# Kernel tuning notes

Hardware: AMD Instinct MI355X
Metric: run time of the kernel (lower is better)

## Reference

```python
import jax, jax.numpy as jnp
import numpy as np

HEADS = 8
GROUPS = 32   # Group_cnt in the source
WIN = 16      # config.local_window_size


def _gn_nc(x, groups, eps):
    # group_norm on [N, C] (affine=False)
    N, C = x.shape
    xg = x.reshape(N, groups, C // groups)
    m = xg.mean(axis=2, keepdims=True)
    v = xg.var(axis=2, keepdims=True)
    return ((xg - m) / jnp.sqrt(v + eps)).reshape(N, C)


def _gn_nchw(x, groups, eps):
    # group_norm on [B, C, H, W] (affine=False)
    B, C, H, W = x.shape
    xg = x.reshape(B, groups, C // groups, H, W)
    m = xg.mean(axis=(2, 3, 4), keepdims=True)
    v = xg.var(axis=(2, 3, 4), keepdims=True)
    return ((xg - m) / jnp.sqrt(v + eps)).reshape(B, C, H, W)


def _conv3x3(x, w, b=None):
    y = jax.lax.conv_general_dilated(x, w, (1, 1), 'SAME',
                                     dimension_numbers=('NCHW', 'OIHW', 'NCHW'))
    return y if b is None else y + b[None, :, None, None]


def _forward(x, temb, conv1_w, conv1_b, conv2_w, g_diff, g_res, g2, g3,
             qkv2_w, qkv2_b, out2_w, qkv3_w, qkv3_b, out3_w,
             lsa_qkv_w, lsa_out_w):
    # ---- Residual_Block (layer1) ----
    h = _gn_nchw(x, GROUPS, 1e-6)
    h = _conv3x3(h, conv1_w, conv1_b)
    h = h + g_diff * temb[:, :, None, None]      # gate_diffusion (ReZero-style gate)
    h = jax.nn.silu(h)
    h = _gn_nchw(h, GROUPS, 1e-6)
    h = _conv3x3(h, conv2_w)
    h = _gn_nchw(h, GROUPS, 1e-6)
    x = x + g_res * h                            # gate_residual

    B, C, Fq, T = x.shape
    Dh = C // HEADS
    scale = 1.0 / jnp.sqrt(jnp.float32(Dh))      # (F/heads)**0.5 divisor

    # ---- SelfAttention over frequency axis (layer2): batch B*T, seq Fq ----
    xf = x.transpose(0, 3, 2, 1).reshape(B * T, Fq, C)
    qkv = xf @ qkv2_w + qkv2_b                   # [B*T, Fq, 3C]
    q, k, v = [t.reshape(B * T, Fq, HEADS, Dh) for t in jnp.split(qkv, 3, axis=-1)]
    p = jax.nn.softmax(jnp.einsum('bLhf,blhf->bLlh', q, k) * scale, axis=2)
    y = jnp.einsum('blhf,bLlh->bLhf', v, p).reshape(B * T, Fq, C) @ out2_w
    y = _gn_nc(y.reshape(-1, C), GROUPS, 1e-5).reshape(B * T, Fq, C)
    xf = xf + g2 * y                             # gate2

    # ---- GlobalAttention over time axis (layer3): batch B*Fq, seq T ----
    xt = xf.reshape(B, T, Fq, C).transpose(0, 2, 1, 3).reshape(B * Fq, T, C)
    qkv = xt @ qkv3_w + qkv3_b
    q, k, v = [t.reshape(B * Fq, T, HEADS, Dh) for t in jnp.split(qkv, 3, axis=-1)]
    p = jax.nn.softmax(jnp.einsum('bhf,blhf->blh', q.mean(axis=1), k) * scale, axis=1)
    y = jnp.einsum('blhf,blh->bhf', v, p).reshape(B * Fq, C) @ out3_w
    y = _gn_nc(y, GROUPS, 1e-5).reshape(B * Fq, 1, C)
    xt = xt + g3 * y                             # gate3, broadcast over T
    x = xt.reshape(B, Fq, T, C).transpose(0, 3, 1, 2)

    # ---- LSA_block (layer4): pre-norm local windowed attention along T, residual ----
    h = _gn_nchw(x, GROUPS, 1e-5)
    h = h.transpose(0, 2, 3, 1).reshape(B * Fq, T, C)
    nw = T // WIN
    qkv = (h @ lsa_qkv_w).reshape(B * Fq, nw, WIN, 3 * C)
    q, k, v = [t.reshape(B * Fq, nw, WIN, HEADS, Dh) for t in jnp.split(qkv, 3, axis=-1)]
    p = jax.nn.softmax(jnp.einsum('nwqhd,nwkhd->nwqkh', q, k) * scale, axis=3)
    o = jnp.einsum('nwqkh,nwkhd->nwqhd', p, v).reshape(B * Fq, T, C) @ lsa_out_w
    return x + o.reshape(B, Fq, T, C).transpose(0, 3, 1, 2)


def setup_inputs() -> dict:
    key = jax.random.key(0)
    ks = jax.random.split(key, 10)
    B, C, Fq, T = 4, 256, 64, 256
    w = lambda k, s: jax.random.normal(k, s, dtype=jnp.float32) * 0.02
    return {
        'x': jax.random.normal(ks[0], (B, C, Fq, T), dtype=jnp.float32),
        'temb': jax.random.normal(ks[1], (B, C), dtype=jnp.float32),
        'conv1_w': w(ks[2], (C, C, 3, 3)),
        'conv1_b': jnp.zeros((C,), jnp.float32),
        'conv2_w': w(ks[3], (C, C, 3, 3)),
        'g_diff': jnp.full((1,), 0.5, jnp.float32),
        'g_res': jnp.full((1,), 0.5, jnp.float32),
        'g2': jnp.full((1,), 0.5, jnp.float32),
        'g3': jnp.full((1,), 0.5, jnp.float32),
        'qkv2_w': w(ks[4], (C, 3 * C)),
        'qkv2_b': jnp.zeros((3 * C,), jnp.float32),
        'out2_w': w(ks[5], (C, C)),
        'qkv3_w': w(ks[6], (C, 3 * C)),
        'qkv3_b': jnp.zeros((3 * C,), jnp.float32),
        'out3_w': w(ks[7], (C, C)),
        'lsa_qkv_w': w(ks[8], (C, 3 * C)),
        'lsa_out_w': w(ks[9], (C, C)),
    }


def reference(x, temb, conv1_w, conv1_b, conv2_w, g_diff, g_res, g2, g3,
              qkv2_w, qkv2_b, out2_w, qkv3_w, qkv3_b, out3_w,
              lsa_qkv_w, lsa_out_w):
    return _forward(x, temb, conv1_w, conv1_b, conv2_w, g_diff, g_res, g2, g3,
                    qkv2_w, qkv2_b, out2_w, qkv3_w, qkv3_b, out3_w,
                    lsa_qkv_w, lsa_out_w)
```

## Files before the change

### kernel.cpp

```cpp
#include <hip/hip_runtime.h>

#define NN 16777216
#define CC 256
#define FF 64
#define TT 256

typedef short v8s __attribute__((ext_vector_type(8)));
typedef float v4f __attribute__((ext_vector_type(4)));

__device__ __forceinline__ unsigned short f2bf(float f) {
  unsigned u = __float_as_uint(f);
  u += 0x7fff + ((u >> 16) & 1);
  return (unsigned short)(u >> 16);
}
__device__ __forceinline__ float bf2f(unsigned short h) {
  return __uint_as_float(((unsigned)h) << 16);
}
__device__ __forceinline__ unsigned packbf2(float a, float b) {
  return (unsigned)f2bf(a) | ((unsigned)f2bf(b) << 16);
}
__device__ __forceinline__ void unpack8(uint4 u, float* d) {
  d[0] = __uint_as_float(u.x << 16); d[1] = __uint_as_float(u.x & 0xffff0000u);
  d[2] = __uint_as_float(u.y << 16); d[3] = __uint_as_float(u.y & 0xffff0000u);
  d[4] = __uint_as_float(u.z << 16); d[5] = __uint_as_float(u.z & 0xffff0000u);
  d[6] = __uint_as_float(u.w << 16); d[7] = __uint_as_float(u.w & 0xffff0000u);
}

__device__ __forceinline__ void blockReduce2(float& a, float& b, float* sbuf) {
  #pragma unroll
  for (int off = 32; off > 0; off >>= 1) {
    a += __shfl_down(a, off, 64);
    b += __shfl_down(b, off, 64);
  }
  int w = threadIdx.x >> 6;
  if ((threadIdx.x & 63) == 0) { sbuf[w] = a; sbuf[4 + w] = b; }
  __syncthreads();
  if (threadIdx.x == 0) {
    a = sbuf[0] + sbuf[1] + sbuf[2] + sbuf[3];
    b = sbuf[4] + sbuf[5] + sbuf[6] + sbuf[7];
  }
}

__global__ void prep_all_k(const float* __restrict__ c1w, const float* __restrict__ c2w,
    const float* __restrict__ q2w, const float* __restrict__ o2w, const float* __restrict__ q3w,
    const float* __restrict__ lqw, const float* __restrict__ low,
    unsigned short* __restrict__ WB1, unsigned short* __restrict__ WB2,
    unsigned short* __restrict__ Q2T, unsigned short* __restrict__ O2T,
    unsigned short* __restrict__ Q3T, unsigned short* __restrict__ LQT,
    unsigned short* __restrict__ LOT, float* __restrict__ stats) {
  long s = (long)blockIdx.x * 256 + threadIdx.x;
  if (s < 1024) { stats[s] = 0.f; return; }
  s -= 1024;
  if (s < 589824) {
    int co = (int)(s / 2304), r = (int)(s % 2304);
    int ci = r / 9, tap = r % 9;
    WB1[(tap * 256 + co) * 256 + ci] = f2bf(c1w[s]);
    return;
  }
  s -= 589824;
  if (s < 589824) {
    int co = (int)(s / 2304), r = (int)(s % 2304);
    int ci = r / 9, tap = r % 9;
    WB2[(tap * 256 + co) * 256 + ci] = f2bf(c2w[s]);
    return;
  }
  s -= 589824;
  if (s < 196608) { int k = (int)(s / 768), n = (int)(s % 768); Q2T[n * 256 + k] = f2bf(q2w[s]); return; }
  s -= 196608;
  if (s < 65536)  { int k = (int)(s / 256), n = (int)(s % 256); O2T[n * 256 + k] = f2bf(o2w[s]); return; }
  s -= 65536;
  if (s < 196608) { int k = (int)(s / 768), n = (int)(s % 768); Q3T[n * 256 + k] = f2bf(q3w[s]); return; }
  s -= 196608;
  if (s < 196608) { int k = (int)(s / 768), n = (int)(s % 768); LQT[n * 256 + k] = f2bf(lqw[s]); return; }
  s -= 196608;
  if (s < 65536)  { int k = (int)(s / 256), n = (int)(s % 256); LOT[n * 256 + k] = f2bf(low[s]); return; }
}

__global__ __launch_bounds__(256) void gn_stats_contig(const float* __restrict__ src, float* __restrict__ stats) {
  __shared__ float sbuf[8];
  int grp = blockIdx.x >> 3, chunk = blockIdx.x & 7;
  const float4* p = (const float4*)src + grp * 32768 + chunk * 4096;
  float s = 0.f, ss = 0.f;
  for (int i = threadIdx.x; i < 4096; i += 256) {
    float4 v = p[i];
    s += v.x + v.y + v.z + v.w;
    ss += v.x * v.x + v.y * v.y + v.z * v.z + v.w * v.w;
  }
  blockReduce2(s, ss, sbuf);
  if (threadIdx.x == 0) { atomicAdd(&stats[grp], s); atomicAdd(&stats[128 + grp], ss); }
}

__global__ __launch_bounds__(256) void gn_apply_tr_k(const float* __restrict__ src,
    const float* __restrict__ stats, unsigned short* __restrict__ XC, float eps) {
  __shared__ float sT[32][33];
  int bx = blockIdx.x;
  int r = bx >> 6;
  int c0 = ((bx >> 3) & 7) * 32;
  int t0 = (bx & 7) * 32;
  int b = r >> 6, f = r & 63;
  int tl = threadIdx.x & 31, tr = threadIdx.x >> 5;
  #pragma unroll
  for (int i = 0; i < 4; ++i) {
    int c = c0 + tr + i * 8;
    int grp = b * 32 + (c >> 3);
    float mean = stats[grp] * (1.f / 131072.f);
    float var = stats[128 + grp] * (1.f / 131072.f) - mean * mean;
    float rv = rsqrtf(var + eps);
    float v = src[((b * 256 + c) * 64 + f) * 256 + t0 + tl];
    sT[tr + i * 8][tl] = (v - mean) * rv;
  }
  __syncthreads();
  #pragma unroll
  for (int i = 0; i < 4; ++i) {
    int t = t0 + tr + i * 8;
    XC[(((size_t)(b * 64 + f)) * 256 + t) * 256 + c0 + tl] = f2bf(sT[tl][tr + i * 8]);
  }
}

__global__ __launch_bounds__(256) void gn_tr_resid_k(const float* __restrict__ h,
    const float* __restrict__ x, const float* __restrict__ stats,
    const float* __restrict__ gate, float* __restrict__ XF, float eps) {
  __shared__ float sT[32][33];
  int bx = blockIdx.x;
  int r = bx >> 6;
  int c0 = ((bx >> 3) & 7) * 32;
  int t0 = (bx & 7) * 32;
  int b = r >> 6, f = r & 63;
  int tl = threadIdx.x & 31, tr = threadIdx.x >> 5;
  float g = gate[0];
  #pragma unroll
  for (int i = 0; i < 4; ++i) {
    int c = c0 + tr + i * 8;
    int grp = b * 32 + (c >> 3);
    float mean = stats[grp] * (1.f / 131072.f);
    float var = stats[128 + grp] * (1.f / 131072.f) - mean * mean;
    float rv = rsqrtf(var + eps);
    int idx = ((b * 256 + c) * 64 + f) * 256 + t0 + tl;
    sT[tr + i * 8][tl] = x[idx] + g * (h[idx] - mean) * rv;
  }
  __syncthreads();
  #pragma unroll
  for (int i = 0; i < 4; ++i) {
    int t = t0 + tr + i * 8;
    XF[(((size_t)(b * 256 + t)) * 64 + f) * 256 + c0 + tl] = sT[tl][tr + i * 8];
  }
}

__global__ __launch_bounds__(256, 4) void conv3x3_mfma_k(const unsigned short* __restrict__ XC,
    const unsigned short* __restrict__ wb, const float* __restrict__ bias,
    const float* __restrict__ temb, const float* __restrict__ gd,
    float* __restrict__ out, float* __restrict__ ostats, int mode) {
  __shared__ __align__(16) unsigned short sIn[258][40];
  __shared__ __align__(16) unsigned short sW[3][64][40];
  int f  = blockIdx.x;
  int b  = blockIdx.y >> 2;
  int co0 = (blockIdx.y & 3) * 64;
  int tid = threadIdx.x;
  int wave = tid >> 6, lane = tid & 63;
  int lm = lane & 15, quad = lane >> 4;
  int w64 = wave * 64;
  v4f acc[4][4];
  #pragma unroll
  for (int i = 0; i < 4; ++i)
    #pragma unroll
    for (int j = 0; j < 4; ++j) acc[i][j] = (v4f)(0.f);

  for (int ci0 = 0; ci0 < 256; ci0 += 32) {
    for (int df = 0; df < 3; ++df) {
      __syncthreads();
      for (int s = tid; s < 1032; s += 256) {
        int tl = s >> 2, part = s & 3;
        int fi = f + df - 1, tg = tl - 1;
        uint4 val = make_uint4(0, 0, 0, 0);
        if (fi >= 0 && fi < 64 && tg >= 0 && tg < 256)
          val = *(const uint4*)&XC[(((size_t)(b * 64 + fi)) * 256 + tg) * 256 + ci0 + part * 8];
        *(uint4*)&sIn[tl][part * 8] = val;
      }
      for (int s = tid; s < 768; s += 256) {
        int tap3 = s >> 8, r = s & 255;
        int co = r >> 2, part = r & 3;
        *(uint4*)&sW[tap3][co][part * 8] =
            *(const uint4*)&wb[((size_t)((df * 3 + tap3) * 256) + co0 + co) * 256 + ci0 + part * 8];
      }
      __syncthreads();
      #pragma unroll
      for (int dt = 0; dt < 3; ++dt) {
        v8s A[4];
        #pragma unroll
        for (int mt = 0; mt < 4; ++mt)
          A[mt] = *(const v8s*)&sIn[w64 + mt * 16 + lm + dt][quad * 8];
        #pragma unroll
        for (int nt = 0; nt < 4; ++nt) {
          v8s B = *(const v8s*)&sW[dt][nt * 16 + lm][quad * 8];
          #pragma unroll
          for (int mt = 0; mt < 4; ++mt)
            acc[mt][nt] = __builtin_amdgcn_mfma_f32_16x16x32_bf16(A[mt], B, acc[mt][nt], 0, 0, 0);
        }
      }
    }
  }
  __syncthreads();
  float* sStat = (float*)sIn;
  float gdv = mode ? gd[0] : 0.f;
  float sch, qch;
  #pragma unroll
  for (int nt = 0; nt < 4; ++nt) {
    int co = co0 + nt * 16 + lm;
    float bb = 0.f;
    if (mode) bb = bias[co] + gdv * temb[b * 256 + co];
    sch = 0.f; qch = 0.f;
    #pragma unroll
    for (int mt = 0; mt < 4; ++mt) {
      int t = w64 + mt * 16 + quad * 4;
      float v0 = acc[mt][nt][0] + bb, v1 = acc[mt][nt][1] + bb;
      float v2 = acc[mt][nt][2] + bb, v3 = acc[mt][nt][3] + bb;
      if (mode) {
        v0 = v0 / (1.f + expf(-v0)); v1 = v1 / (1.f + expf(-v1));
        v2 = v2 / (1.f + expf(-v2)); v3 = v3 / (1.f + expf(-v3));
      }
      float4 o; o.x = v0; o.y = v1; o.z = v2; o.w = v3;
      *(float4*)&out[(((size_t)b * 256 + co) * 64 + f) * 256 + t] = o;
      sch += v0 + v1 + v2 + v3;
      qch += v0 * v0 + v1 * v1 + v2 * v2 + v3 * v3;
    }
    sch += __shfl_xor(sch, 16); qch += __shfl_xor(qch, 16);
    sch += __shfl_xor(sch, 32); qch += __shfl_xor(qch, 32);
    if (quad == 0) {
      sStat[((wave * 4 + nt) * 16 + lm) * 2]     = sch;
      sStat[((wave * 4 + nt) * 16 + lm) * 2 + 1] = qch;
    }
  }
  __syncthreads();
  if (tid < 64) {
    int c = tid;
    int nt = c >> 4, lmm = c & 15;
    float s = 0.f, q = 0.f;
    #pragma unroll
    for (int w = 0; w < 4; ++w) {
      s += sStat[((w * 4 + nt) * 16 + lmm) * 2];
      q += sStat[((w * 4 + nt) * 16 + lmm) * 2 + 1];
    }
    s += __shfl_xor(s, 1); q += __shfl_xor(q, 1);
    s += __shfl_xor(s, 2); q += __shfl_xor(q, 2);
    s += __shfl_xor(s, 4); q += __shfl_xor(q, 4);
    if ((c & 7) == 0) {
      int g = (co0 + c) >> 3;
      atomicAdd(&ostats[b * 32 + g], s);
      atomicAdd(&ostats[128 + b * 32 + g], q);
    }
  }
}

__global__ __launch_bounds__(256) void gemm_af32_k(const float* __restrict__ A, int lda,
    const unsigned short* __restrict__ BT, const float* __restrict__ bias,
    unsigned short* __restrict__ Cb, int ldc,
    const float* __restrict__ gstats, int growbase, float eps) {
  __shared__ __align__(16) unsigned short sA[128][40];
  __shared__ __align__(16) unsigned short sB[128][40];
  int n0 = blockIdx.x * 128, m0 = blockIdx.y * 128;
  int tid = threadIdx.x;
  int wave = tid >> 6, lane = tid & 63;
  int wm = wave >> 1, wn = wave & 1;
  int lm = lane & 15, quad = lane >> 4;
  v4f acc[4][4];
  #pragma unroll
  for (int i = 0; i < 4; ++i)
    #pragma unroll
    for (int j = 0; j < 4; ++j) acc[i][j] = (v4f)(0.f);

  for (int k0 = 0; k0 < 256; k0 += 32) {
    __syncthreads();
    #pragma unroll
    for (int i = 0; i < 4; ++i) {
      int s = tid + i * 256;
      int row = s >> 3, k4 = s & 7;
      float4 av = *(const float4*)&A[(size_t)(m0 + row) * lda + k0 + k4 * 4];
      if (gstats) {
        int grp = ((growbase + m0 + row) >> 14) * 32 + ((k0 + k4 * 4) >> 3);
        float mean = gstats[grp] * (1.f / 131072.f);
        float var = gstats[128 + grp] * (1.f / 131072.f) - mean * mean;
        float rr = rsqrtf(var + eps);
        av.x = (av.x - mean) * rr; av.y = (av.y - mean) * rr;
        av.z = (av.z - mean) * rr; av.w = (av.w - mean) * rr;
      }
      *(uint2*)&sA[row][k4 * 4] = make_uint2(packbf2(av.x, av.y), packbf2(av.z, av.w));
    }
    #pragma unroll
    for (int i = 0; i < 2; ++i) {
      int s = tid + i * 256;
      int n = s >> 2, part = s & 3;
      *(uint4*)&sB[n][part * 8] = *(const uint4*)&BT[(size_t)(n0 + n) * 256 + k0 + part * 8];
    }
    __syncthreads();
    v8s Af[4];
    #pragma unroll
    for (int mt = 0; mt < 4; ++mt)
      Af[mt] = *(const v8s*)&sA[wm * 64 + mt * 16 + lm][quad * 8];
    #pragma unroll
    for (int nt = 0; nt < 4; ++nt) {
      v8s Bf = *(const v8s*)&sB[wn * 64 + nt * 16 + lm][quad * 8];
      #pragma unroll
      for (int mt = 0; mt < 4; ++mt)
        acc[mt][nt] = __builtin_amdgcn_mfma_f32_16x16x32_bf16(Af[mt], Bf, acc[mt][nt], 0, 0, 0);
    }
  }
  #pragma unroll
  for (int nt = 0; nt < 4; ++nt) {
    int col = n0 + wn * 64 + nt * 16 + lm;
    float bb = bias ? bias[col] : 0.f;
    #pragma unroll
    for (int mt = 0; mt < 4; ++mt) {
      int row = m0 + wm * 64 + mt * 16 + quad * 4;
      #pragma unroll
      for (int r = 0; r < 4; ++r)
        Cb[(size_t)(row + r) * ldc + col] = f2bf(acc[mt][nt][r] + bb);
    }
  }
}

__global__ __launch_bounds__(256) void gemm_abf16_k(const unsigned short* __restrict__ A, int lda,
    const unsigned short* __restrict__ BT,
    const float* __restrict__ xfin, float* __restrict__ xtout, int rowbase,
    unsigned short* __restrict__ Cb, int ldc, const float* __restrict__ gate, int mode) {
  __shared__ __align__(16) unsigned short sA[128][40];
  __shared__ __align__(16) unsigned short sB[128][40];
  int n0 = blockIdx.x * 128, m0 = blockIdx.y * 128;
  int tid = threadIdx.x;
  int wave = tid >> 6, lane = tid & 63;
  int wm = wave >> 1, wn = wave & 1;
  int lm = lane & 15, quad = lane >> 4;
  v4f acc[4][4];
  #pragma unroll
  for (int i = 0; i < 4; ++i)
    #pragma unroll
    for (int j = 0; j < 4; ++j) acc[i][j] = (v4f)(0.f);

  for (int k0 = 0; k0 < 256; k0 += 32) {
    __syncthreads();
    #pragma unroll
    for (int i = 0; i < 2; ++i) {
      int s = tid + i * 256;
      int row = s >> 2, part = s & 3;
      *(uint4*)&sA[row][part * 8] = *(const uint4*)&A[(size_t)(m0 + row) * lda + k0 + part * 8];
      *(uint4*)&sB[row][part * 8] = *(const uint4*)&BT[(size_t)(n0 + row) * 256 + k0 + part * 8];
    }
    __syncthreads();
    v8s Af[4];
    #pragma unroll
    for (int mt = 0; mt < 4; ++mt)
      Af[mt] = *(const v8s*)&sA[wm * 64 + mt * 16 + lm][quad * 8];
    #pragma unroll
    for (int nt = 0; nt < 4; ++nt) {
      v8s Bf = *(const v8s*)&sB[wn * 64 + nt * 16 + lm][quad * 8];
      #pragma unroll
      for (int mt = 0; mt < 4; ++mt)
        acc[mt][nt] = __builtin_amdgcn_mfma_f32_16x16x32_bf16(Af[mt], Bf, acc[mt][nt], 0, 0, 0);
    }
  }
  if (mode == 1) {
    float g = gate[0];
    #pragma unroll
    for (int mt = 0; mt < 4; ++mt) {
      int rowb = m0 + wm * 64 + mt * 16 + quad * 4;
      #pragma unroll
      for (int r = 0; r < 4; ++r) {
        int rowl = rowb + r;
        int rowg = rowbase + rowl;
        int b = rowg >> 14, t = (rowg >> 6) & 255, fq = rowg & 63;
        size_t xtrow = (size_t)((b * 64 + fq) * 256 + t) * 256;
        #pragma unroll
        for (int nt = 0; nt < 4; ++nt) {
          float v = acc[mt][nt][r];
          float s = v, q = v * v;
          s += __shfl_xor(s, 1); q += __shfl_xor(q, 1);
          s += __shfl_xor(s, 2); q += __shfl_xor(q, 2);
          s += __shfl_xor(s, 4); q += __shfl_xor(q, 4);
          float m = s * 0.125f;
          float var = q * 0.125f - m * m;
          float norm = (v - m) * rsqrtf(var + 1e-5f);
          int col = n0 + wn * 64 + nt * 16 + lm;
          xtout[xtrow + col] = xfin[(size_t)rowl * 256 + col] + g * norm;
        }
      }
    }
  } else if (mode == 2) {
    #pragma unroll
    for (int mt = 0; mt < 4; ++mt) {
      int rowb = m0 + wm * 64 + mt * 16 + quad * 4;
      #pragma unroll
      for (int r = 0; r < 4; ++r) {
        int rowl = rowb + r;
        int rowg = rowbase + rowl;
        int b = rowg >> 14, fq = (rowg >> 8) & 63, t = rowg & 255;
        #pragma unroll
        for (int nt = 0; nt < 4; ++nt) {
          int col = n0 + wn * 64 + nt * 16 + lm;
          float v = acc[mt][nt][r] + xfin[(size_t)rowl * 256 + col];
          xtout[(((size_t)b * 256 + col) * 64 + fq) * 256 + t] = v;
        }
      }
    }
  } else {
    #pragma unroll
    for (int nt = 0; nt < 4; ++nt) {
      int col = n0 + wn * 64 + nt * 16 + lm;
      #pragma unroll
      for (int mt = 0; mt < 4; ++mt) {
        int row = m0 + wm * 64 + mt * 16 + quad * 4;
        #pragma unroll
        for (int r = 0; r < 4; ++r)
          Cb[(size_t)(row + r) * ldc + col] = f2bf(acc[mt][nt][r]);
      }
    }
  }
}

__global__ __launch_bounds__(256) void gemm_k(const float* __restrict__ A, int lda,
    const float* __restrict__ Bm, int N, const float* __restrict__ bias,
    float* __restrict__ Cm, int ldc, int gn) {
  __shared__ __align__(16) float sA[16][64];
  __shared__ __align__(16) float sB[16][64];
  int n0 = blockIdx.x * 64, m0 = blockIdx.y * 64;
  int tid = threadIdx.x;
  int tx = tid & 15, ty = tid >> 4;
  int arow = m0 + (tid >> 2), acol = (tid & 3) * 4;
  int brow = tid >> 4, bcol = (tid & 15) * 4;
  float acc[4][4] = {};
  for (int k0 = 0; k0 < 256; k0 += 16) {
    __syncthreads();
    float4 av = *(const float4*)&A[(size_t)arow * lda + k0 + acol];
    sA[acol + 0][tid >> 2] = av.x;
    sA[acol + 1][tid >> 2] = av.y;
    sA[acol + 2][tid >> 2] = av.z;
    sA[acol + 3][tid >> 2] = av.w;
    *(float4*)&sB[brow][bcol] = *(const float4*)&Bm[(k0 + brow) * N + n0 + bcol];
    __syncthreads();
    #pragma unroll
    for (int kk = 0; kk < 16; ++kk) {
      float4 a = *(const float4*)&sA[kk][ty * 4];
      float4 b = *(const float4*)&sB[kk][tx * 4];
      float aa[4] = {a.x, a.y, a.z, a.w};
      float bb[4] = {b.x, b.y, b.z, b.w};
      #pragma unroll
      for (int i = 0; i < 4; ++i)
        #pragma unroll
        for (int j = 0; j < 4; ++j)
          acc[i][j] += aa[i] * bb[j];
    }
  }
  #pragma unroll
  for (int i = 0; i < 4; ++i) {
    float m = 0.f, rv = 1.f;
    if (gn) {
      float s = acc[i][0] + acc[i][1] + acc[i][2] + acc[i][3];
      float q = acc[i][0] * acc[i][0] + acc[i][1] * acc[i][1]
              + acc[i][2] * acc[i][2] + acc[i][3] * acc[i][3];
      s += __shfl_xor(s, 1); q += __shfl_xor(q, 1);
      m = s * 0.125f;
      float var = q * 0.125f - m * m;
      rv = rsqrtf(var + 1e-5f);
    }
    #pragma unroll
    for (int j = 0; j < 4; ++j) {
      int n = n0 + tx * 4 + j;
      float v = acc[i][j];
      if (gn) v = (v - m) * rv;
      else if (bias) v += bias[n];
      Cm[(size_t)(m0 + ty * 4 + i) * ldc + n] = v;
    }
  }
}

__global__ __launch_bounds__(256) void attn2_mfma_k(unsigned short* __restrict__ Q) {
  __shared__ __align__(16) unsigned short sP[4][64][72];
  __shared__ __align__(16) unsigned short sVt[4][32][72];
  int bt = blockIdx.x;
  int tid = threadIdx.x;
  int wave = tid >> 6, lane = tid & 63;
  int lm = lane & 15, quad = lane >> 4;
  const float scale = 0.17677669529663687f;
  size_t rowbase = (size_t)bt * 64;
  unsigned short (*P)[72] = sP[wave];
  unsigned short (*Vt)[72] = sVt[wave];
  #pragma unroll
  for (int hh = 0; hh < 2; ++hh) {
    int h = wave * 2 + hh;
    int hoff = h * 32;
    v8s Af[4], Bf[4];
    #pragma unroll
    for (int mt = 0; mt < 4; ++mt)
      Af[mt] = *(const v8s*)&Q[(rowbase + mt * 16 + lm) * 768 + hoff + quad * 8];
    #pragma unroll
    for (int nt = 0; nt < 4; ++nt)
      Bf[nt] = *(const v8s*)&Q[(rowbase + nt * 16 + lm) * 768 + 256 + hoff + quad * 8];
    v4f S[4][4];
    #pragma unroll
    for (int mt = 0; mt < 4; ++mt)
      #pragma unroll
      for (int nt = 0; nt < 4; ++nt)
        S[mt][nt] = __builtin_amdgcn_mfma_f32_16x16x32_bf16(Af[mt], Bf[nt], (v4f)(0.f), 0, 0, 0);
    #pragma unroll
    for (int part = 0; part < 4; ++part) {
      uint4 u = *(const uint4*)&Q[(rowbase + lane) * 768 + 512 + hoff + part * 8];
      unsigned short* up = (unsigned short*)&u;
      #pragma unroll
      for (int j = 0; j < 8; ++j) Vt[part * 8 + j][lane] = up[j];
    }
    float inv[4][4];
    #pragma unroll
    for (int mt = 0; mt < 4; ++mt) {
      #pragma unroll
      for (int r = 0; r < 4; ++r) {
        float v0 = S[mt][0][r] * scale, v1 = S[mt][1][r] * scale;
        float v2 = S[mt][2][r] * scale, v3 = S[mt][3][r] * scale;
        float mx = fmaxf(fmaxf(v0, v1), fmaxf(v2, v3));
        mx = fmaxf(mx, __shfl_xor(mx, 1));
        mx = fmaxf(mx, __shfl_xor(mx, 2));
        mx = fmaxf(mx, __shfl_xor(mx, 4));
        mx = fmaxf(mx, __shfl_xor(mx, 8));
        float e0 = __expf(v0 - mx), e1 = __expf(v1 - mx);
        float e2 = __expf(v2 - mx), e3 = __expf(v3 - mx);
        float sm = e0 + e1 + e2 + e3;
        sm += __shfl_xor(sm, 1);
        sm += __shfl_xor(sm, 2);
        sm += __shfl_xor(sm, 4);
        sm += __shfl_xor(sm, 8);
        inv[mt][r] = 1.f / sm;
        int row = mt * 16 + quad * 4 + r;
        P[row][lm]      = f2bf(e0);
        P[row][16 + lm] = f2bf(e1);
        P[row][32 + lm] = f2bf(e2);
        P[row][48 + lm] = f2bf(e3);
      }
    }
    v8s Ap[4][2], Bv[2][2];
    #pragma unroll
    for (int mt = 0; mt < 4; ++mt)
      #pragma unroll
      for (int kc = 0; kc < 2; ++kc)
        Ap[mt][kc] = *(const v8s*)&P[mt * 16 + lm][kc * 32 + quad * 8];
    #pragma unroll
    for (int nd = 0; nd < 2; ++nd)
      #pragma unroll
      for (int kc = 0; kc < 2; ++kc)
        Bv[nd][kc] = *(const v8s*)&Vt[nd * 16 + lm][kc * 32 + quad * 8];
    #pragma unroll
    for (int mt = 0; mt < 4; ++mt) {
      #pragma unroll
      for (int nd = 0; nd < 2; ++nd) {
        v4f O = (v4f)(0.f);
        O = __builtin_amdgcn_mfma_f32_16x16x32_bf16(Ap[mt][0], Bv[nd][0], O, 0, 0, 0);
        O = __builtin_amdgcn_mfma_f32_16x16x32_bf16(Ap[mt][1], Bv[nd][1], O, 0, 0, 0);
        #pragma unroll
        for (int r = 0; r < 4; ++r)
          P[mt * 16 + quad * 4 + r][nd * 16 + lm] = f2bf(O[r] * inv[mt][r]);
      }
    }
    #pragma unroll
    for (int part = 0; part < 4; ++part) {
      uint4 u = *(const uint4*)&P[lane][part * 8];
      *(uint4*)&Q[(rowbase + lane) * 768 + hoff + part * 8] = u;
    }
  }
}

__global__ __launch_bounds__(256) void attn3_k(const unsigned short* __restrict__ Q3,
                                               float* __restrict__ y3, int bf_base) {
  __shared__ float sQp[64][33];
  __shared__ float sqm[32];
  __shared__ float sp[256];
  __shared__ float sred[256];
  int bfl = blockIdx.x >> 3, h = blockIdx.x & 7;
  int tid = threadIdx.x;
  int tq = tid >> 2, c4 = tid & 3;
  int d8 = c4 * 8;
  const float scale = 0.17677669529663687f;
  size_t rowbase = (size_t)bfl * 256;
  {
    float a[8] = {};
    #pragma unroll
    for (int i = 0; i < 4; ++i) {
      int t = i * 64 + tq;
      float v[8];
      unpack8(*(const uint4*)&Q3[(rowbase + t) * 768 + h * 32 + d8], v);
      #pragma unroll
      for (int j = 0; j < 8; ++j) a[j] += v[j];
    }
    #pragma unroll
    for (int j = 0; j < 8; ++j) sQp[tq][d8 + j] = a[j];
  }
  __syncthreads();
  if (tid < 32) {
    float m = 0.f;
    for (int g = 0; g < 64; ++g) m += sQp[g][tid];
    sqm[tid] = m * (1.f / 256.f);
  }
  __syncthreads();
  {
    float dot = 0.f;
    #pragma unroll
    for (int p = 0; p < 4; ++p) {
      float v[8];
      unpack8(*(const uint4*)&Q3[(rowbase + tid) * 768 + 256 + h * 32 + p * 8], v);
      #pragma unroll
      for (int j = 0; j < 8; ++j) dot += sqm[p * 8 + j] * v[j];
    }
    sp[tid] = dot * scale;
    sred[tid] = sp[tid];
  }
  __syncthreads();
  for (int st = 128; st > 0; st >>= 1) { if (tid < st) sred[tid] = fmaxf(sred[tid], sred[tid + st]); __syncthreads(); }
  float mx = sred[0];
  __syncthreads();
  float e = expf(sp[tid] - mx);
  sred[tid] = e;
  __syncthreads();
  for (int st = 128; st > 0; st >>= 1) { if (tid < st) sred[tid] += sred[tid + st]; __syncthreads(); }
  float rinv = 1.f / sred[0];
  sp[tid] = e * rinv;
  __syncthreads();
  {
    float a[8] = {};
    #pragma unroll
    for (int i = 0; i < 4; ++i) {
      int t = i * 64 + tq;
      float w = sp[t];
      float v[8];
      unpack8(*(const uint4*)&Q3[(rowbase + t) * 768 + 512 + h * 32 + d8], v);
      #pragma unroll
      for (int j = 0; j < 8; ++j) a[j] += w * v[j];
    }
    #pragma unroll
    for (int j = 0; j < 8; ++j) sQp[tq][d8 + j] = a[j];
  }
  __syncthreads();
  if (tid < 32) {
    float o = 0.f;
    for (int g = 0; g < 64; ++g) o += sQp[g][tid];
    y3[(size_t)(bf_base + bfl) * 256 + h * 32 + tid] = o;
  }
}

__global__ __launch_bounds__(256) void lsa_attn_k(unsigned short* __restrict__ Q4) {
  __shared__ __align__(16) float sX[16][772];
  __shared__ float sS[8][16][17];
  __shared__ float sInv[8][16];
  int bfl = blockIdx.x >> 4, w = blockIdx.x & 15;
  int tid = threadIdx.x;
  size_t rb = ((size_t)(bfl * 256 + w * 16)) * 768;
  for (int s = tid; s < 1536; s += 256) {
    int t = s / 96, c8 = (s - t * 96) * 8;
    unpack8(*(const uint4*)&Q4[rb + t * 768 + c8], &sX[t][c8]);
  }
  __syncthreads();
  const float scale = 0.17677669529663687f;
  #pragma unroll
  for (int rep = 0; rep < 8; ++rep) {
    int idx = tid + rep * 256;
    int h = idx >> 8, q = (idx >> 4) & 15, k = idx & 15;
    float dot = 0.f;
    const float* qp = &sX[q][h * 32];
    const float* kp = &sX[k][256 + h * 32];
    for (int d = 0; d < 32; ++d) dot += qp[d] * kp[d];
    sS[h][q][k] = dot * scale;
  }
  __syncthreads();
  if (tid < 128) {
    int h = tid >> 4, q = tid & 15;
    float mx = -1e30f;
    for (int k = 0; k < 16; ++k) mx = fmaxf(mx, sS[h][q][k]);
    float sum = 0.f;
    for (int k = 0; k < 16; ++k) { float e = expf(sS[h][q][k] - mx); sS[h][q][k] = e; sum += e; }
    sInv[h][q] = 1.f / sum;
  }
  __syncthreads();
  #pragma unroll
  for (int rep = 0; rep < 8; ++rep) {
    int idx = tid + rep * 256;
    int t = idx >> 7, c2 = (idx & 127) * 2;
    int h = c2 >> 5;
    float a0 = 0.f, a1 = 0.f;
    for (int k = 0; k < 16; ++k) {
      float p = sS[h][t][k];
      a0 += p * sX[k][512 + c2];
      a1 += p * sX[k][512 + c2 + 1];
    }
    float riv = sInv[h][t];
    *(unsigned*)&Q4[rb + t * 768 + c2] = packbf2(a0 * riv, a1 * riv);
  }
}

__global__ __launch_bounds__(256) void bcast_add_k(float* __restrict__ XT, const float* __restrict__ y3n,
                                                   const float* __restrict__ gate) {
  int i4 = blockIdx.x * 256 + threadIdx.x;
  int flat = i4 * 4;
  int r = flat >> 16, c = flat & 255;
  float g = gate[0];
  float4 v = ((float4*)XT)[i4];
  float4 a = *(const float4*)&y3n[r * 256 + c];
  v.x += g * a.x; v.y += g * a.y; v.z += g * a.z; v.w += g * a.w;
  ((float4*)XT)[i4] = v;
}

__global__ __launch_bounds__(256) void gn_stats_xt2_k(const float* __restrict__ X, float* __restrict__ stats) {
  __shared__ float sacc[4][64];
  int bf = blockIdx.x >> 1, half = blockIdx.x & 1;
  int b = bf >> 6;
  int tid = threadIdx.x;
  const float4* p = (const float4*)X + (size_t)bf * 16384 + half * 8192;
  float s = 0.f, q = 0.f;
  #pragma unroll 4
  for (int k = 0; k < 32; ++k) {
    float4 v = p[tid + k * 256];
    s += v.x + v.y + v.z + v.w;
    q += v.x * v.x + v.y * v.y + v.z * v.z + v.w * v.w;
  }
  s += __shfl_xor(s, 1); q += __shfl_xor(q, 1);
  int lane = tid & 63, wave = tid >> 6;
  if ((lane & 1) == 0) {
    int g = (lane >> 1) & 31;
    sacc[wave][g * 2] = s;
    sacc[wave][g * 2 + 1] = q;
  }
  __syncthreads();
  if (tid < 64) {
    int g = tid >> 1, isq = tid & 1;
    float acc = sacc[0][g * 2 + isq] + sacc[1][g * 2 + isq]
              + sacc[2][g * 2 + isq] + sacc[3][g * 2 + isq];
    atomicAdd(&stats[isq * 128 + b * 32 + g], acc);
  }
}

extern "C" void kernel_launch(void* const* d_in, const int* in_sizes, int n_in,
                              void* d_out, int out_size, void* d_ws, size_t ws_size,
                              hipStream_t stream) {
  (void)in_sizes; (void)n_in; (void)out_size;
  const float* x        = (const float*)d_in[0];
  const float* temb     = (const float*)d_in[1];
  const float* conv1_w  = (const float*)d_in[2];
  const float* conv1_b  = (const float*)d_in[3];
  const float* conv2_w  = (const float*)d_in[4];
  const float* g_diff   = (const float*)d_in[5];
  const float* g_res    = (const float*)d_in[6];
  const float* g2       = (const float*)d_in[7];
  const float* g3       = (const float*)d_in[8];
  const float* qkv2_w   = (const float*)d_in[9];
  const float* qkv2_b   = (const float*)d_in[10];
  const float* out2_w   = (const float*)d_in[11];
  const float* qkv3_w   = (const float*)d_in[12];
  const float* qkv3_b   = (const float*)d_in[13];
  const float* out3_w   = (const float*)d_in[14];
  const float* lsa_qkv_w = (const float*)d_in[15];
  const float* lsa_out_w = (const float*)d_in[16];
  float* out = (float*)d_out;
  float* ws = (float*)d_ws;

  int NCHv = 4;
  {
    auto need = [](int nch) -> size_t {
      size_t rows = 65536 / nch;
      size_t uslots = rows * 512;
      if (uslots < 8388608) uslots = 8388608;
      return 4ull * ((size_t)NN + uslots + 950272 + 198000);
    };
    if (ws_size >= need(1)) NCHv = 1;
    else if (ws_size >= need(2)) NCHv = 2;
  }
  const size_t rows = 65536 / NCHv;

  float* W = ws;
  float* U = ws + (size_t)NN;
  unsigned short* XC  = (unsigned short*)U;
  unsigned short* QB  = (unsigned short*)U;
  size_t uslots = rows * 512; if (uslots < 8388608) uslots = 8388608;
  float* WREG = U + uslots;
  unsigned short* WB1   = (unsigned short*)WREG;
  unsigned short* WB2   = WB1 + 589824;
  unsigned short* QKV2T = WB2 + 589824;
  unsigned short* OUT2T = QKV2T + 196608;
  unsigned short* QKV3T = OUT2T + 65536;
  unsigned short* LSAQT = QKV3T + 196608;
  unsigned short* LSAOT = LSAQT + 196608;
  float* Y3    = WREG + 950272;
  float* Y3O   = Y3 + 65536;
  float* Y3N   = Y3O + 65536;
  float* STATS = Y3N + 65536;
  float* ST0 = STATS, *ST1 = STATS + 256, *ST2 = STATS + 512, *ST3 = STATS + 768;
  float* D = out;

  dim3 b256(256);
  prep_all_k<<<7428, b256, 0, stream>>>(conv1_w, conv2_w, qkv2_w, out2_w, qkv3_w,
                                        lsa_qkv_w, lsa_out_w,
                                        WB1, WB2, QKV2T, OUT2T, QKV3T, LSAQT, LSAOT, STATS);

  gn_stats_contig<<<1024, b256, 0, stream>>>(x, ST0);
  gn_apply_tr_k<<<16384, b256, 0, stream>>>(x, ST0, XC, 1e-6f);
  conv3x3_mfma_k<<<dim3(64, 16), b256, 0, stream>>>(XC, WB1, conv1_b, temb, g_diff, W, ST1, 1);
  gn_apply_tr_k<<<16384, b256, 0, stream>>>(W, ST1, XC, 1e-6f);
  conv3x3_mfma_k<<<dim3(64, 16), b256, 0, stream>>>(XC, WB2, nullptr, nullptr, nullptr, W, ST2, 0);
  gn_tr_resid_k<<<16384, b256, 0, stream>>>(W, x, ST2, g_res, D, 1e-6f);

  for (int c = 0; c < NCHv; ++c) {
    float* XFr = D + (size_t)c * rows * 256;
    gemm_af32_k<<<dim3(6, rows / 128), b256, 0, stream>>>(XFr, 256, QKV2T, qkv2_b, QB, 768, nullptr, 0, 0.f);
    attn2_mfma_k<<<rows / 64, b256, 0, stream>>>(QB);
    gemm_abf16_k<<<dim3(2, rows / 128), b256, 0, stream>>>(QB, 768, OUT2T,
                                                           XFr, W, (int)(c * rows),
                                                           nullptr, 256, g2, 1);
  }

  for (int c = 0; c < NCHv; ++c) {
    const float* XTr = W + (size_t)c * rows * 256;
    gemm_af32_k<<<dim3(6, rows / 128), b256, 0, stream>>>(XTr, 256, QKV3T, qkv3_b, QB, 768, nullptr, 0, 0.f);
    attn3_k<<<(rows / 256) * 8, b256, 0, stream>>>(QB, Y3, c * (int)(rows / 256));
  }
  gemm_k<<<dim3(4, 4), b256, 0, stream>>>(Y3, 256, out3_w, 256, nullptr, Y3N, 256, 1);
  bcast_add_k<<<16384, b256, 0, stream>>>(W, Y3N, g3);

  gn_stats_xt2_k<<<512, b256, 0, stream>>>(W, ST3);
  for (int c = 0; c < NCHv; ++c) {
    const float* XTr = W + (size_t)c * rows * 256;
    gemm_af32_k<<<dim3(6, rows / 128), b256, 0, stream>>>(XTr, 256, LSAQT, nullptr, QB, 768,
                                                          ST3, (int)(c * rows), 1e-5f);
    lsa_attn_k<<<(rows / 256) * 16, b256, 0, stream>>>(QB);
    gemm_abf16_k<<<dim3(2, rows / 128), b256, 0, stream>>>(QB, 768, LSAOT,
                                                           XTr, out, (int)(c * rows),
                                                           nullptr, 256, nullptr, 2);
  }
}
```

Before: 1.005 ms.

## Fuse query column-sum into QKV3 GEMM epilogue and merge broadcast-add with GN stats

The QKV3 GEMM now accumulates per-sequence query column sums with atomics in its epilogue and skips writing the Q block to memory, so attn3 reads the precomputed mean instead of rereading 256 Q rows. Separately, the gated broadcast add and the group-norm statistics pass over the time-major tensor are merged into one kernel, which removes one full read/write sweep of the 64 MB buffer. This adds atomic contention on qsum and relies on the mean-only use of Q in attn3.

```diff
diff --git a/kernel.cpp b/kernel.cpp
--- a/kernel.cpp
+++ b/kernel.cpp
@@ -47,7 +47,8 @@
     unsigned short* __restrict__ WB1, unsigned short* __restrict__ WB2,
     unsigned short* __restrict__ Q2T, unsigned short* __restrict__ O2T,
     unsigned short* __restrict__ Q3T, unsigned short* __restrict__ LQT,
-    unsigned short* __restrict__ LOT, float* __restrict__ stats) {
+    unsigned short* __restrict__ LOT, float* __restrict__ stats,
+    float* __restrict__ qsum) {
   long s = (long)blockIdx.x * 256 + threadIdx.x;
   if (s < 1024) { stats[s] = 0.f; return; }
   s -= 1024;
@@ -74,6 +75,8 @@
   if (s < 196608) { int k = (int)(s / 768), n = (int)(s % 768); LQT[n * 256 + k] = f2bf(lqw[s]); return; }
   s -= 196608;
   if (s < 65536)  { int k = (int)(s / 256), n = (int)(s % 256); LOT[n * 256 + k] = f2bf(low[s]); return; }
+  s -= 65536;
+  if (s < 65536)  { qsum[s] = 0.f; }
 }
 
 __global__ __launch_bounds__(256) void gn_stats_contig(const float* __restrict__ src, float* __restrict__ stats) {
@@ -254,7 +257,8 @@
 __global__ __launch_bounds__(256) void gemm_af32_k(const float* __restrict__ A, int lda,
     const unsigned short* __restrict__ BT, const float* __restrict__ bias,
     unsigned short* __restrict__ Cb, int ldc,
-    const float* __restrict__ gstats, int growbase, float eps) {
+    const float* __restrict__ gstats, int growbase, float eps,
+    float* __restrict__ qsum, int qrowbase) {
   __shared__ __align__(16) unsigned short sA[128][40];
   __shared__ __align__(16) unsigned short sB[128][40];
   int n0 = blockIdx.x * 128, m0 = blockIdx.y * 128;
@@ -304,16 +308,36 @@
         acc[mt][nt] = __builtin_amdgcn_mfma_f32_16x16x32_bf16(Af[mt], Bf, acc[mt][nt], 0, 0, 0);
     }
   }
-  #pragma unroll
-  for (int nt = 0; nt < 4; ++nt) {
-    int col = n0 + wn * 64 + nt * 16 + lm;
-    float bb = bias ? bias[col] : 0.f;
-    #pragma unroll
-    for (int mt = 0; mt < 4; ++mt) {
-      int row = m0 + wm * 64 + mt * 16 + quad * 4;
-      #pragma unroll
-      for (int r = 0; r < 4; ++r)
-        Cb[(size_t)(row + r) * ldc + col] = f2bf(acc[mt][nt][r] + bb);
+  if (qsum && n0 < 256) {
+    #pragma unroll
+    for (int nt = 0; nt < 4; ++nt) {
+      int col = n0 + wn * 64 + nt * 16 + lm;
+      float bb = bias ? bias[col] : 0.f;
+      float cs = 0.f;
+      #pragma unroll
+      for (int mt = 0; mt < 4; ++mt)
+        #pragma unroll
+        for (int r = 0; r < 4; ++r)
+          cs += acc[mt][nt][r] + bb;
+      cs += __shfl_xor(cs, 16);
+      cs += __shfl_xor(cs, 32);
+      if (quad == 0) {
+        int qrow = (qrowbase + m0) >> 8;
+        atomicAdd(&qsum[(size_t)qrow * 256 + col], cs);
+      }
+    }
+  } else {
+    #pragma unroll
+    for (int nt = 0; nt < 4; ++nt) {
+      int col = n0 + wn * 64 + nt * 16 + lm;
+      float bb = bias ? bias[col] : 0.f;
+      #pragma unroll
+      for (int mt = 0; mt < 4; ++mt) {
+        int row = m0 + wm * 64 + mt * 16 + quad * 4;
+        #pragma unroll
+        for (int r = 0; r < 4; ++r)
+          Cb[(size_t)(row + r) * ldc + col] = f2bf(acc[mt][nt][r] + bb);
+      }
     }
   }
 }
@@ -565,6 +589,7 @@
 }
 
 __global__ __launch_bounds__(256) void attn3_k(const unsigned short* __restrict__ Q3,
+                                               const float* __restrict__ qsum,
                                                float* __restrict__ y3, int bf_base) {
   __shared__ float sQp[64][33];
   __shared__ float sqm[32];
@@ -576,25 +601,8 @@
   int d8 = c4 * 8;
   const float scale = 0.17677669529663687f;
   size_t rowbase = (size_t)bfl * 256;
-  {
-    float a[8] = {};
-    #pragma unroll
-    for (int i = 0; i < 4; ++i) {
-      int t = i * 64 + tq;
-      float v[8];
-      unpack8(*(const uint4*)&Q3[(rowbase + t) * 768 + h * 32 + d8], v);
-      #pragma unroll
-      for (int j = 0; j < 8; ++j) a[j] += v[j];
-    }
-    #pragma unroll
-    for (int j = 0; j < 8; ++j) sQp[tq][d8 + j] = a[j];
-  }
-  __syncthreads();
-  if (tid < 32) {
-    float m = 0.f;
-    for (int g = 0; g < 64; ++g) m += sQp[g][tid];
-    sqm[tid] = m * (1.f / 256.f);
-  }
+  if (tid < 32)
+    sqm[tid] = qsum[(size_t)(bf_base + bfl) * 256 + h * 32 + tid] * (1.f / 256.f);
   __syncthreads();
   {
     float dot = 0.f;
@@ -690,44 +698,39 @@
   }
 }
 
-__global__ __launch_bounds__(256) void bcast_add_k(float* __restrict__ XT, const float* __restrict__ y3n,
-                                                   const float* __restrict__ gate) {
-  int i4 = blockIdx.x * 256 + threadIdx.x;
-  int flat = i4 * 4;
-  int r = flat >> 16, c = flat & 255;
-  float g = gate[0];
-  float4 v = ((float4*)XT)[i4];
-  float4 a = *(const float4*)&y3n[r * 256 + c];
-  v.x += g * a.x; v.y += g * a.y; v.z += g * a.z; v.w += g * a.w;
-  ((float4*)XT)[i4] = v;
-}
-
-__global__ __launch_bounds__(256) void gn_stats_xt2_k(const float* __restrict__ X, float* __restrict__ stats) {
+__global__ __launch_bounds__(256) void bcast_stats_k(float* __restrict__ XT, const float* __restrict__ y3n,
+                                                     const float* __restrict__ gate, float* __restrict__ stats) {
   __shared__ float sacc[4][64];
   int bf = blockIdx.x >> 1, half = blockIdx.x & 1;
   int b = bf >> 6;
   int tid = threadIdx.x;
-  const float4* p = (const float4*)X + (size_t)bf * 16384 + half * 8192;
+  float4* p = (float4*)XT + (size_t)bf * 16384 + (size_t)half * 8192;
+  int lane = tid & 63, wave = tid >> 6;
+  float4 a = ((const float4*)y3n)[(size_t)bf * 64 + lane];
+  float g = gate[0];
+  a.x *= g; a.y *= g; a.z *= g; a.w *= g;
   float s = 0.f, q = 0.f;
   #pragma unroll 4
   for (int k = 0; k < 32; ++k) {
-    float4 v = p[tid + k * 256];
+    int idx = tid + k * 256;
+    float4 v = p[idx];
+    v.x += a.x; v.y += a.y; v.z += a.z; v.w += a.w;
+    p[idx] = v;
     s += v.x + v.y + v.z + v.w;
     q += v.x * v.x + v.y * v.y + v.z * v.z + v.w * v.w;
   }
   s += __shfl_xor(s, 1); q += __shfl_xor(q, 1);
-  int lane = tid & 63, wave = tid >> 6;
   if ((lane & 1) == 0) {
-    int g = (lane >> 1) & 31;
-    sacc[wave][g * 2] = s;
-    sacc[wave][g * 2 + 1] = q;
+    int gg = (lane >> 1) & 31;
+    sacc[wave][gg * 2] = s;
+    sacc[wave][gg * 2 + 1] = q;
   }
   __syncthreads();
   if (tid < 64) {
-    int g = tid >> 1, isq = tid & 1;
-    float acc = sacc[0][g * 2 + isq] + sacc[1][g * 2 + isq]
-              + sacc[2][g * 2 + isq] + sacc[3][g * 2 + isq];
-    atomicAdd(&stats[isq * 128 + b * 32 + g], acc);
+    int gg = tid >> 1, isq = tid & 1;
+    float acc = sacc[0][gg * 2 + isq] + sacc[1][gg * 2 + isq]
+              + sacc[2][gg * 2 + isq] + sacc[3][gg * 2 + isq];
+    atomicAdd(&stats[isq * 128 + b * 32 + gg], acc);
   }
 }
 
@@ -782,16 +785,16 @@
   unsigned short* LSAQT = QKV3T + 196608;
   unsigned short* LSAOT = LSAQT + 196608;
   float* Y3    = WREG + 950272;
-  float* Y3O   = Y3 + 65536;
-  float* Y3N   = Y3O + 65536;
+  float* QSUM  = Y3 + 65536;
+  float* Y3N   = QSUM + 65536;
   float* STATS = Y3N + 65536;
   float* ST0 = STATS, *ST1 = STATS + 256, *ST2 = STATS + 512, *ST3 = STATS + 768;
   float* D = out;
 
   dim3 b256(256);
-  prep_all_k<<<7428, b256, 0, stream>>>(conv1_w, conv2_w, qkv2_w, out2_w, qkv3_w,
+  prep_all_k<<<7684, b256, 0, stream>>>(conv1_w, conv2_w, qkv2_w, out2_w, qkv3_w,
                                         lsa_qkv_w, lsa_out_w,
-                                        WB1, WB2, QKV2T, OUT2T, QKV3T, LSAQT, LSAOT, STATS);
+                                        WB1, WB2, QKV2T, OUT2T, QKV3T, LSAQT, LSAOT, STATS, QSUM);
 
   gn_stats_contig<<<1024, b256, 0, stream>>>(x, ST0);
   gn_apply_tr_k<<<16384, b256, 0, stream>>>(x, ST0, XC, 1e-6f);
@@ -802,7 +805,8 @@
 
   for (int c = 0; c < NCHv; ++c) {
     float* XFr = D + (size_t)c * rows * 256;
-    gemm_af32_k<<<dim3(6, rows / 128), b256, 0, stream>>>(XFr, 256, QKV2T, qkv2_b, QB, 768, nullptr, 0, 0.f);
+    gemm_af32_k<<<dim3(6, rows / 128), b256, 0, stream>>>(XFr, 256, QKV2T, qkv2_b, QB, 768,
+                                                          nullptr, 0, 0.f, nullptr, 0);
     attn2_mfma_k<<<rows / 64, b256, 0, stream>>>(QB);
     gemm_abf16_k<<<dim3(2, rows / 128), b256, 0, stream>>>(QB, 768, OUT2T,
                                                            XFr, W, (int)(c * rows),
@@ -811,17 +815,17 @@
 
   for (int c = 0; c < NCHv; ++c) {
     const float* XTr = W + (size_t)c * rows * 256;
-    gemm_af32_k<<<dim3(6, rows / 128), b256, 0, stream>>>(XTr, 256, QKV3T, qkv3_b, QB, 768, nullptr, 0, 0.f);
-    attn3_k<<<(rows / 256) * 8, b256, 0, stream>>>(QB, Y3, c * (int)(rows / 256));
+    gemm_af32_k<<<dim3(6, rows / 128), b256, 0, stream>>>(XTr, 256, QKV3T, qkv3_b, QB, 768,
+                                                          nullptr, 0, 0.f, QSUM, (int)(c * rows));
+    attn3_k<<<(rows / 256) * 8, b256, 0, stream>>>(QB, QSUM, Y3, c * (int)(rows / 256));
   }
   gemm_k<<<dim3(4, 4), b256, 0, stream>>>(Y3, 256, out3_w, 256, nullptr, Y3N, 256, 1);
-  bcast_add_k<<<16384, b256, 0, stream>>>(W, Y3N, g3);
-
-  gn_stats_xt2_k<<<512, b256, 0, stream>>>(W, ST3);
+  bcast_stats_k<<<512, b256, 0, stream>>>(W, Y3N, g3, ST3);
+
   for (int c = 0; c < NCHv; ++c) {
     const float* XTr = W + (size_t)c * rows * 256;
     gemm_af32_k<<<dim3(6, rows / 128), b256, 0, stream>>>(XTr, 256, LSAQT, nullptr, QB, 768,
-                                                          ST3, (int)(c * rows), 1e-5f);
+                                                          ST3, (int)(c * rows), 1e-5f, nullptr, 0);
     lsa_attn_k<<<(rows / 256) * 16, b256, 0, stream>>>(QB);
     gemm_abf16_k<<<dim3(2, rows / 128), b256, 0, stream>>>(QB, 768, LSAOT,
                                                            XTr, out, (int)(c * rows),
```

After: 1.031 ms. +2.6%, slower.
